# Optimization experiments

Measured on AMD Instinct MI355X. Metric: run time of the kernel, lower is better.

## Reference

```python
import jax, jax.numpy as jnp
import numpy as np

DIM = 128

def _layernorm(x, g, b, eps=1e-5):
    mu = jnp.mean(x, axis=-1, keepdims=True)
    var = jnp.var(x, axis=-1, keepdims=True)
    return (x - mu) * jax.lax.rsqrt(var + eps) * g + b

def setup_inputs() -> dict:
    key = jax.random.key(0)
    ks = jax.random.split(key, 12)
    B, T, O, d = 64, 1024, 128, DIM
    s = 1.0 / np.sqrt(d)
    s2 = 1.0 / np.sqrt(2 * d)
    return {
        "token_nodes": jax.random.normal(ks[0], (B, T, d), jnp.float32),
        "obj_nodes": jax.random.normal(ks[1], (B, O, d), jnp.float32),
        "attn_to_obj": jax.random.uniform(ks[2], (B, T, O), jnp.float32),
        "W_msg_o": jax.random.uniform(ks[3], (d, d), jnp.float32, -s, s),
        "b_msg_o": jnp.zeros((d,), jnp.float32),
        "W_msg_t": jax.random.uniform(ks[4], (d, d), jnp.float32, -s, s),
        "b_msg_t": jnp.zeros((d,), jnp.float32),
        "W_upd_t": jax.random.uniform(ks[5], (2 * d, d), jnp.float32, -s2, s2),
        "b_upd_t": jnp.zeros((d,), jnp.float32),
        "W_upd_o": jax.random.uniform(ks[6], (2 * d, d), jnp.float32, -s2, s2),
        "b_upd_o": jnp.zeros((d,), jnp.float32),
        "g_ln_t": jnp.ones((d,), jnp.float32),
        "beta_ln_t": jnp.zeros((d,), jnp.float32),
        "g_ln_o": jnp.ones((d,), jnp.float32),
        "beta_ln_o": jnp.zeros((d,), jnp.float32),
    }

def reference(token_nodes, obj_nodes, attn_to_obj,
              W_msg_o, b_msg_o, W_msg_t, b_msg_t,
              W_upd_t, b_upd_t, W_upd_o, b_upd_o,
              g_ln_t, beta_ln_t, g_ln_o, beta_ln_o):
    # messages from objects -> tokens
    msg_o = obj_nodes @ W_msg_o + b_msg_o                      # [B,O,d]
    agg_to_t = jnp.einsum('bto,bod->btd', attn_to_obj, msg_o)  # [B,T,d]
    # messages from tokens -> objects (transposed attention)
    msg_t = token_nodes @ W_msg_t + b_msg_t                    # [B,T,d]
    agg_to_o = jnp.einsum('bto,btd->bod', attn_to_obj, msg_t)  # [B,O,d]
    # fused update MLPs (dropout is identity in eval mode)
    new_t = jax.nn.relu(jnp.concatenate([token_nodes, agg_to_t], axis=-1) @ W_upd_t + b_upd_t)
    new_o = jax.nn.relu(jnp.concatenate([obj_nodes, agg_to_o], axis=-1) @ W_upd_o + b_upd_o)
    new_t = _layernorm(token_nodes + new_t, g_ln_t, beta_ln_t)
    new_o = _layernorm(obj_nodes + new_o, g_ln_o, beta_ln_o)
    return (new_t, new_o)
```

## Files before the change

### kernel.cpp

```cpp
#include <hip/hip_runtime.h>

typedef unsigned short u16;
typedef __attribute__((ext_vector_type(8))) short bf16x8;
typedef __attribute__((ext_vector_type(4))) float f32x4;

#define NB 64
#define NT 1024
#define NO 128
#define ND 128

__device__ __forceinline__ u16 f2bf(float f) {
    union { float f; unsigned u; } v; v.f = f;
    unsigned r = v.u + 0x7FFFu + ((v.u >> 16) & 1u);
    return (u16)(r >> 16);
}
__device__ __forceinline__ float bf2f(short s) {
    union { unsigned u; float f; } v; v.u = ((unsigned)(u16)s) << 16; return v.f;
}

__device__ __forceinline__ bf16x8 frag_from_f32(const float* p) {
    const float4 a = *reinterpret_cast<const float4*>(p);
    const float4 b = *reinterpret_cast<const float4*>(p + 4);
    bf16x8 r;
    r[0] = (short)f2bf(a.x); r[1] = (short)f2bf(a.y);
    r[2] = (short)f2bf(a.z); r[3] = (short)f2bf(a.w);
    r[4] = (short)f2bf(b.x); r[5] = (short)f2bf(b.y);
    r[6] = (short)f2bf(b.z); r[7] = (short)f2bf(b.w);
    return r;
}

__global__ void k_prep_weights(const float* __restrict__ Wmo, const float* __restrict__ Wmt,
                               const float* __restrict__ Wut, const float* __restrict__ Wuo,
                               u16* __restrict__ WmoT, u16* __restrict__ WmtT,
                               u16* __restrict__ WutT, u16* __restrict__ WuoT) {
    int idx = blockIdx.x * 256 + threadIdx.x;
    if (idx < 16384) {
        int k = idx >> 7, n = idx & 127;
        WmoT[n * 128 + k] = f2bf(Wmo[idx]);
    } else if (idx < 32768) {
        int i = idx - 16384; int k = i >> 7, n = i & 127;
        WmtT[n * 128 + k] = f2bf(Wmt[i]);
    } else if (idx < 65536) {
        int i = idx - 32768; int k = i >> 7, n = i & 127;
        WutT[n * 256 + (k ^ ((n & 7) << 3))] = f2bf(Wut[i]);
    } else if (idx < 98304) {
        int i = idx - 65536; int k = i >> 7, n = i & 127;
        WuoT[n * 256 + k] = f2bf(Wuo[i]);
    }
}

__global__ __launch_bounds__(256, 4)
void k_msg_o(const float* __restrict__ obj, const u16* __restrict__ WmoT,
             const float* __restrict__ bmo, u16* __restrict__ msg_oT) {
    __shared__ u16 lds_m[128][72];
    int bid = blockIdx.x;
    int rows_base = bid * 64;
    int l = threadIdx.x & 63, w = threadIdx.x >> 6;
    int l15 = l & 15, lk = (l >> 4) * 8, rsub = (l >> 4) * 4;
    int wrow = w * 16;
    int row0 = rows_base + wrow;

    f32x4 acc[8] = {};
    const float* xp = obj + (size_t)(row0 + l15) * 128;
#pragma unroll
    for (int kk = 0; kk < 4; kk++) {
        bf16x8 a = frag_from_f32(xp + kk * 32 + lk);
#pragma unroll
        for (int ct = 0; ct < 8; ct++) {
            bf16x8 bfr = *reinterpret_cast<const bf16x8*>(WmoT + (ct * 16 + l15) * 128 + kk * 32 + lk);
            acc[ct] = __builtin_amdgcn_mfma_f32_16x16x32_bf16(a, bfr, acc[ct], 0, 0, 0);
        }
    }
#pragma unroll
    for (int ct = 0; ct < 8; ct++) {
        int n = ct * 16 + l15;
        float bv = bmo[n];
        ushort4 pk;
        pk.x = f2bf(acc[ct][0] + bv);
        pk.y = f2bf(acc[ct][1] + bv);
        pk.z = f2bf(acc[ct][2] + bv);
        pk.w = f2bf(acc[ct][3] + bv);
        *reinterpret_cast<ushort4*>(&lds_m[n][wrow + rsub]) = pk;
    }
    __syncthreads();
    int n = threadIdx.x >> 1, h = threadIdx.x & 1;
    const u16* src = &lds_m[n][h * 32];
    int b = rows_base >> 7, o0 = rows_base & 127;
    u16* rowp = msg_oT + (size_t)(b * 128 + n) * 128;
#pragma unroll
    for (int i = 0; i < 4; i++) {
        int off = o0 + h * 32 + i * 8;
        *reinterpret_cast<bf16x8*>(rowp + (off ^ ((n & 7) << 3))) =
            *reinterpret_cast<const bf16x8*>(src + i * 8);
    }
}

__global__ __launch_bounds__(512, 2)
void k_P(const float* __restrict__ attn, const float* __restrict__ tok,
         u16* __restrict__ Psl, float* __restrict__ rs_part) {
    __shared__ u16 aT[128 * 256];
    __shared__ u16 dT[128 * 256];
    int b = blockIdx.x >> 2, ks = blockIdx.x & 3;
    int kb = ks * 256;
    int tid = threadIdx.x;

    int og = (tid & 31) * 4;
    int tg = tid >> 5;
    const float* asrc = attn + ((size_t)b * NT + kb) * 128;
    const float* tsrc = tok  + ((size_t)b * NT + kb) * 128;
#pragma unroll
    for (int half = 0; half < 2; half++) {
        const float* src = half ? tsrc : asrc;
        u16* buf = half ? dT : aT;
#pragma unroll
        for (int c = 0; c < 2; c++) {
            int t0 = tg * 16 + c * 8;
            f32x4 v[8];
#pragma unroll
            for (int i = 0; i < 8; i++)
                v[i] = *reinterpret_cast<const f32x4*>(src + (size_t)(t0 + i) * 128 + og);
            int gr = t0 >> 3;
#pragma unroll
            for (int j = 0; j < 4; j++) {
                int o = og + j;
                bf16x8 pk;
#pragma unroll
                for (int i = 0; i < 8; i++) pk[i] = (short)f2bf(v[i][j]);
                *reinterpret_cast<bf16x8*>(&buf[o * 256 + ((gr ^ (o & 31)) << 3)]) = pk;
            }
        }
    }
    __syncthreads();

    int l = tid & 63, w = tid >> 6;
    int l15 = l & 15, lk = (l >> 4) * 8, rsub = (l >> 4) * 4;
    int ro = w * 16 + l15;
    f32x4 acc[8] = {};
    float rsum = 0.f;
#pragma unroll
    for (int kk = 0; kk < 8; kk++) {
        int tt = kk * 32 + lk;
        bf16x8 a = *reinterpret_cast<const bf16x8*>(&aT[ro * 256 + (((tt >> 3) ^ (ro & 31)) << 3)]);
#pragma unroll
        for (int i = 0; i < 8; i++) rsum += bf2f(a[i]);
#pragma unroll
        for (int ct = 0; ct < 8; ct++) {
            int d = ct * 16 + l15;
            bf16x8 bf = *reinterpret_cast<const bf16x8*>(&dT[d * 256 + (((tt >> 3) ^ (d & 31)) << 3)]);
            acc[ct] = __builtin_amdgcn_mfma_f32_16x16x32_bf16(a, bf, acc[ct], 0, 0, 0);
        }
    }
    rsum += __shfl_xor(rsum, 16, 64);
    rsum += __shfl_xor(rsum, 32, 64);
    if (l < 16) rs_part[((size_t)ks * NB + b) * NO + w * 16 + l15] = rsum;
    u16* pout = Psl + (((size_t)(ks * NB + b)) * NO + w * 16) * ND;
#pragma unroll
    for (int ct = 0; ct < 8; ct++)
#pragma unroll
        for (int r = 0; r < 4; r++)
            pout[(size_t)(rsub + r) * ND + ct * 16 + l15] = f2bf(acc[ct][r]);
}

__global__ __launch_bounds__(256, 4)
void k_obj_final(const float* __restrict__ obj, const u16* __restrict__ Psl,
                 const float* __restrict__ rs_part, const u16* __restrict__ WmtT,
                 const float* __restrict__ bmt, const u16* __restrict__ WuoT,
                 const float* __restrict__ buo, const float* __restrict__ g,
                 const float* __restrict__ beta, float* __restrict__ out) {
    __shared__ u16 P_lds[32][136];
    __shared__ u16 agg_lds[32][136];
    __shared__ float rs_lds[32];
    __shared__ float part_s[32][2], part_sq[32][2];
    int bid = blockIdx.x;
    int b = bid >> 2, ot = bid & 3;
    int ob = ot * 32;
    int tid = threadIdx.x;
    {
        int row = tid >> 3, c0 = (tid & 7) * 16;
        float sm[16];
#pragma unroll
        for (int i = 0; i < 16; i++) sm[i] = 0.f;
#pragma unroll
        for (int ks = 0; ks < 4; ks++) {
            const u16* p = Psl + (((size_t)(ks * NB + b)) * NO + ob + row) * ND + c0;
            bf16x8 v0 = *reinterpret_cast<const bf16x8*>(p);
            bf16x8 v1 = *reinterpret_cast<const bf16x8*>(p + 8);
#pragma unroll
            for (int i = 0; i < 8; i++) { sm[i] += bf2f(v0[i]); sm[8 + i] += bf2f(v1[i]); }
        }
#pragma unroll
        for (int j = 0; j < 4; j++) {
            ushort4 pk;
            pk.x = f2bf(sm[j * 4 + 0]); pk.y = f2bf(sm[j * 4 + 1]);
            pk.z = f2bf(sm[j * 4 + 2]); pk.w = f2bf(sm[j * 4 + 3]);
            *reinterpret_cast<ushort4*>(&P_lds[row][c0 + j * 4]) = pk;
        }
        if (tid < 32) {
            float r = 0.f;
#pragma unroll
            for (int ks = 0; ks < 4; ks++) r += rs_part[((size_t)ks * NB + b) * NO + ob + tid];
            rs_lds[tid] = r;
        }
    }
    __syncthreads();
    int l = tid & 63, w = tid >> 6;
    int l15 = l & 15, lk = (l >> 4) * 8, rsub = (l >> 4) * 4;
    int wr = (w & 1) * 16, wc = (w >> 1) * 64;
    f32x4 agg[4] = {};
#pragma unroll
    for (int kk = 0; kk < 4; kk++) {
        bf16x8 a = *reinterpret_cast<const bf16x8*>(&P_lds[wr + l15][kk * 32 + lk]);
#pragma unroll
        for (int ct = 0; ct < 4; ct++) {
            bf16x8 bf = *reinterpret_cast<const bf16x8*>(WmtT + (wc + ct * 16 + l15) * 128 + kk * 32 + lk);
            agg[ct] = __builtin_amdgcn_mfma_f32_16x16x32_bf16(a, bf, agg[ct], 0, 0, 0);
        }
    }
#pragma unroll
    for (int ct = 0; ct < 4; ct++) {
        int n = wc + ct * 16 + l15;
        float bb = bmt[n];
#pragma unroll
        for (int r = 0; r < 4; r++) {
            float v = agg[ct][r] + rs_lds[wr + rsub + r] * bb;
            agg_lds[wr + rsub + r][n] = f2bf(v);
        }
    }
    __syncthreads();
    f32x4 accm[4] = {};
    const float* objp = obj + ((size_t)(b * NO) + ob + wr + l15) * ND;
#pragma unroll
    for (int kk = 0; kk < 8; kk++) {
        int k0 = kk * 32;
        bf16x8 a = (k0 < 128) ? frag_from_f32(objp + k0 + lk)
                              : *reinterpret_cast<const bf16x8*>(&agg_lds[wr + l15][k0 - 128 + lk]);
#pragma unroll
        for (int ct = 0; ct < 4; ct++) {
            bf16x8 bf = *reinterpret_cast<const bf16x8*>(WuoT + (wc + ct * 16 + l15) * 256 + k0 + lk);
            accm[ct] = __builtin_amdgcn_mfma_f32_16x16x32_bf16(a, bf, accm[ct], 0, 0, 0);
        }
    }
    const float* objr = obj + ((size_t)(b * NO) + ob) * ND;
    float s[4] = {0.f, 0.f, 0.f, 0.f}, sq[4] = {0.f, 0.f, 0.f, 0.f};
#pragma unroll
    for (int ct = 0; ct < 4; ct++) {
        int n = wc + ct * 16 + l15;
        float bv = buo[n];
#pragma unroll
        for (int r = 0; r < 4; r++) {
            int lr = wr + rsub + r;
            float v = objr[(size_t)lr * ND + n] + fmaxf(accm[ct][r] + bv, 0.f);
            accm[ct][r] = v;
            s[r] += v;
            sq[r] += v * v;
        }
    }
#pragma unroll
    for (int ofs = 1; ofs < 16; ofs <<= 1) {
#pragma unroll
        for (int r = 0; r < 4; r++) {
            s[r]  += __shfl_xor(s[r], ofs, 64);
            sq[r] += __shfl_xor(sq[r], ofs, 64);
        }
    }
    if (l15 < 4) {
        float sv = (l15 == 0) ? s[0] : (l15 == 1) ? s[1] : (l15 == 2) ? s[2] : s[3];
        float qv = (l15 == 0) ? sq[0] : (l15 == 1) ? sq[1] : (l15 == 2) ? sq[2] : sq[3];
        part_s[wr + rsub + l15][w >> 1] = sv;
        part_sq[wr + rsub + l15][w >> 1] = qv;
    }
    __syncthreads();
    float mu[4], rstd[4];
#pragma unroll
    for (int r = 0; r < 4; r++) {
        int lr = wr + rsub + r;
        float st = part_s[lr][0] + part_s[lr][1];
        float qt = part_sq[lr][0] + part_sq[lr][1];
        mu[r] = st * (1.f / 128.f);
        rstd[r] = rsqrtf(qt * (1.f / 128.f) - mu[r] * mu[r] + 1e-5f);
    }
#pragma unroll
    for (int ct = 0; ct < 4; ct++) {
        int n = wc + ct * 16 + l15;
        float gn = g[n], bn = beta[n];
#pragma unroll
        for (int r = 0; r < 4; r++) {
            int lr = wr + rsub + r;
            out[((size_t)(b * NO) + ob + lr) * ND + n] = (accm[ct][r] - mu[r]) * rstd[r] * gn + bn;
        }
    }
}

__global__ __launch_bounds__(512, 2)
void k_token_update(const float* __restrict__ tok, const float* __restrict__ attn,
                    const u16* __restrict__ msg_oT, const u16* __restrict__ WutT,
                    const float* __restrict__ bupd, const float* __restrict__ g,
                    const float* __restrict__ beta, float* __restrict__ out) {
    __shared__ u16 msg_lds[16384];
    __shared__ u16 wut_lds[32768];
    __shared__ u16 agg_b[8][16][136];
    int b = blockIdx.x >> 2, bq = blockIdx.x & 3;
    int tid = threadIdx.x;
    {
        const u16* msrc = msg_oT + (size_t)b * 16384;
#pragma unroll
        for (int i = 0; i < 4; i++) {
            int idx = (i * 512 + tid) * 8;
            *reinterpret_cast<bf16x8*>(&msg_lds[idx]) = *reinterpret_cast<const bf16x8*>(msrc + idx);
        }
#pragma unroll
        for (int i = 0; i < 8; i++) {
            int idx = (i * 512 + tid) * 8;
            *reinterpret_cast<bf16x8*>(&wut_lds[idx]) = *reinterpret_cast<const bf16x8*>(WutT + idx);
        }
    }
    __syncthreads();
    int l = tid & 63, w = tid >> 6;
    int l15 = l & 15, lk = (l >> 4) * 8, rsub = (l >> 4) * 4;

#pragma unroll
    for (int pass = 0; pass < 2; pass++) {
        int trow = bq * 256 + pass * 128 + w * 16;
        size_t rbase = (size_t)b * NT + trow;

        const float* aF = attn + (rbase + l15) * NO;
        bf16x8 af[4];
#pragma unroll
        for (int kk = 0; kk < 4; kk++)
            af[kk] = frag_from_f32(aF + kk * 32 + lk);
        f32x4 acc[8] = {};
#pragma unroll
        for (int kk = 0; kk < 4; kk++) {
#pragma unroll
            for (int ct = 0; ct < 8; ct++) {
                int n = ct * 16 + l15;
                bf16x8 bf = *reinterpret_cast<const bf16x8*>(
                    &msg_lds[n * 128 + ((kk * 32 + lk) ^ ((n & 7) << 3))]);
                acc[ct] = __builtin_amdgcn_mfma_f32_16x16x32_bf16(af[kk], bf, acc[ct], 0, 0, 0);
            }
        }
#pragma unroll
        for (int ct = 0; ct < 8; ct++) {
            int n = ct * 16 + l15;
#pragma unroll
            for (int r = 0; r < 4; r++)
                agg_b[w][rsub + r][n] = f2bf(acc[ct][r]);
        }
        asm volatile("s_waitcnt lgkmcnt(0)" ::: "memory");
        __builtin_amdgcn_sched_barrier(0);
        const float* tokp = tok + (rbase + l15) * ND;
        bf16x8 am[8];
#pragma unroll
        for (int kk = 0; kk < 4; kk++)
            am[kk] = frag_from_f32(tokp + kk * 32 + lk);
#pragma unroll
        for (int kk = 0; kk < 4; kk++)
            am[4 + kk] = *reinterpret_cast<const bf16x8*>(&agg_b[w][l15][kk * 32 + lk]);
        f32x4 accm[8] = {};
#pragma unroll
        for (int kk = 0; kk < 8; kk++) {
#pragma unroll
            for (int ct = 0; ct < 8; ct++) {
                int n = ct * 16 + l15;
                bf16x8 bf = *reinterpret_cast<const bf16x8*>(
                    &wut_lds[n * 256 + ((kk * 32 + lk) ^ ((n & 7) << 3))]);
                accm[ct] = __builtin_amdgcn_mfma_f32_16x16x32_bf16(am[kk], bf, accm[ct], 0, 0, 0);
            }
        }
        const float* tokr = tok + rbase * ND;
        float s[4] = {0.f, 0.f, 0.f, 0.f}, sq[4] = {0.f, 0.f, 0.f, 0.f};
#pragma unroll
        for (int ct = 0; ct < 8; ct++) {
            int n = ct * 16 + l15;
            float bv = bupd[n];
#pragma unroll
            for (int r = 0; r < 4; r++) {
                float v = tokr[(size_t)(rsub + r) * ND + n] + fmaxf(accm[ct][r] + bv, 0.f);
                accm[ct][r] = v;
                s[r] += v;
                sq[r] += v * v;
            }
        }
#pragma unroll
        for (int ofs = 1; ofs < 16; ofs <<= 1) {
#pragma unroll
            for (int r = 0; r < 4; r++) {
                s[r]  += __shfl_xor(s[r], ofs, 64);
                sq[r] += __shfl_xor(sq[r], ofs, 64);
            }
        }
        float mu[4], rstd[4];
#pragma unroll
        for (int r = 0; r < 4; r++) {
            mu[r] = s[r] * (1.f / 128.f);
            rstd[r] = rsqrtf(sq[r] * (1.f / 128.f) - mu[r] * mu[r] + 1e-5f);
        }
#pragma unroll
        for (int ct = 0; ct < 8; ct++) {
            int n = ct * 16 + l15;
            float gn = g[n], bn = beta[n];
#pragma unroll
            for (int r = 0; r < 4; r++)
                out[(rbase + rsub + r) * ND + n] = (accm[ct][r] - mu[r]) * rstd[r] * gn + bn;
        }
    }
}

extern "C" void kernel_launch(void* const* d_in, const int* in_sizes, int n_in,
                              void* d_out, int out_size, void* d_ws, size_t ws_size,
                              hipStream_t stream) {
    const float* tok  = (const float*)d_in[0];
    const float* obj  = (const float*)d_in[1];
    const float* attn = (const float*)d_in[2];
    const float* Wmo  = (const float*)d_in[3];
    const float* bmo  = (const float*)d_in[4];
    const float* Wmt  = (const float*)d_in[5];
    const float* bmt  = (const float*)d_in[6];
    const float* Wut  = (const float*)d_in[7];
    const float* but  = (const float*)d_in[8];
    const float* Wuo  = (const float*)d_in[9];
    const float* buo  = (const float*)d_in[10];
    const float* gt   = (const float*)d_in[11];
    const float* bt   = (const float*)d_in[12];
    const float* go   = (const float*)d_in[13];
    const float* bo   = (const float*)d_in[14];
    float* out = (float*)d_out;

    u16* ws = (u16*)d_ws;
    u16* msg_oT = ws;
    u16* WmoT   = msg_oT + 1048576;
    u16* WmtT   = WmoT + 16384;
    u16* WutT   = WmtT + 16384;
    u16* WuoT   = WutT + 32768;
    u16* Psl    = WuoT + 32768;
    float* rs_part = (float*)(Psl + 4194304);

    k_prep_weights<<<dim3(384), dim3(256), 0, stream>>>(Wmo, Wmt, Wut, Wuo, WmoT, WmtT, WutT, WuoT);
    k_msg_o<<<dim3(128), dim3(256), 0, stream>>>(obj, WmoT, bmo, msg_oT);
    k_P<<<dim3(256), dim3(512), 0, stream>>>(attn, tok, Psl, rs_part);
    k_token_update<<<dim3(256), dim3(512), 0, stream>>>(tok, attn, msg_oT, WutT, but, gt, bt, out);
    k_obj_final<<<dim3(256), dim3(256), 0, stream>>>(obj, Psl, rs_part, WmtT, bmt, WuoT, buo, go, bo,
                                                     out + (size_t)NB * NT * ND);
}
```

Baseline: 65.40 us.

## Fuse weight prep into msg_o kernel and chunk k_P LDS staging

Removes the separate weight-conversion kernel. Each k_msg_o block now converts Wmo into a shared-memory transposed tile, and the blocks together convert the other three weights, saving one launch. k_P now stages its 256-token slice in two 128-token chunks with half the LDS, so launch bounds can request 4 blocks per SM for more occupancy. The cost is an extra barrier per chunk and redundant per-block Wmo conversion work.

```diff
diff --git a/kernel.cpp b/kernel.cpp
--- a/kernel.cpp
+++ b/kernel.cpp
@@ -29,33 +29,40 @@
     return r;
 }
 
-__global__ void k_prep_weights(const float* __restrict__ Wmo, const float* __restrict__ Wmt,
-                               const float* __restrict__ Wut, const float* __restrict__ Wuo,
-                               u16* __restrict__ WmoT, u16* __restrict__ WmtT,
-                               u16* __restrict__ WutT, u16* __restrict__ WuoT) {
-    int idx = blockIdx.x * 256 + threadIdx.x;
-    if (idx < 16384) {
-        int k = idx >> 7, n = idx & 127;
-        WmoT[n * 128 + k] = f2bf(Wmo[idx]);
-    } else if (idx < 32768) {
-        int i = idx - 16384; int k = i >> 7, n = i & 127;
-        WmtT[n * 128 + k] = f2bf(Wmt[i]);
-    } else if (idx < 65536) {
-        int i = idx - 32768; int k = i >> 7, n = i & 127;
-        WutT[n * 256 + (k ^ ((n & 7) << 3))] = f2bf(Wut[i]);
-    } else if (idx < 98304) {
-        int i = idx - 65536; int k = i >> 7, n = i & 127;
-        WuoT[n * 256 + k] = f2bf(Wuo[i]);
-    }
-}
-
 __global__ __launch_bounds__(256, 4)
-void k_msg_o(const float* __restrict__ obj, const u16* __restrict__ WmoT,
-             const float* __restrict__ bmo, u16* __restrict__ msg_oT) {
+void k_msg_o(const float* __restrict__ obj, const float* __restrict__ Wmo,
+             const float* __restrict__ bmo,
+             const float* __restrict__ Wmt, const float* __restrict__ Wut,
+             const float* __restrict__ Wuo,
+             u16* __restrict__ msg_oT, u16* __restrict__ WmtT,
+             u16* __restrict__ WutT, u16* __restrict__ WuoT) {
+    __shared__ u16 wT[128][136];
     __shared__ u16 lds_m[128][72];
     int bid = blockIdx.x;
+    int tid = threadIdx.x;
+
+    for (int idx = bid * 256 + tid; idx < 81920; idx += 32768) {
+        if (idx < 16384) {
+            int k = idx >> 7, n = idx & 127;
+            WmtT[n * 128 + k] = f2bf(Wmt[idx]);
+        } else if (idx < 49152) {
+            int i2 = idx - 16384; int k = i2 >> 7, n = i2 & 127;
+            WutT[n * 256 + (k ^ ((n & 7) << 3))] = f2bf(Wut[i2]);
+        } else {
+            int i2 = idx - 49152; int k = i2 >> 7, n = i2 & 127;
+            WuoT[n * 256 + k] = f2bf(Wuo[i2]);
+        }
+    }
+#pragma unroll
+    for (int i = 0; i < 64; i++) {
+        int idx = i * 256 + tid;
+        int k = idx >> 7, n = idx & 127;
+        wT[n][k] = f2bf(Wmo[idx]);
+    }
+    __syncthreads();
+
     int rows_base = bid * 64;
-    int l = threadIdx.x & 63, w = threadIdx.x >> 6;
+    int l = tid & 63, w = tid >> 6;
     int l15 = l & 15, lk = (l >> 4) * 8, rsub = (l >> 4) * 4;
     int wrow = w * 16;
     int row0 = rows_base + wrow;
@@ -67,7 +74,7 @@
         bf16x8 a = frag_from_f32(xp + kk * 32 + lk);
 #pragma unroll
         for (int ct = 0; ct < 8; ct++) {
-            bf16x8 bfr = *reinterpret_cast<const bf16x8*>(WmoT + (ct * 16 + l15) * 128 + kk * 32 + lk);
+            bf16x8 bfr = *reinterpret_cast<const bf16x8*>(&wT[ct * 16 + l15][kk * 32 + lk]);
             acc[ct] = __builtin_amdgcn_mfma_f32_16x16x32_bf16(a, bfr, acc[ct], 0, 0, 0);
         }
     }
@@ -83,7 +90,7 @@
         *reinterpret_cast<ushort4*>(&lds_m[n][wrow + rsub]) = pk;
     }
     __syncthreads();
-    int n = threadIdx.x >> 1, h = threadIdx.x & 1;
+    int n = tid >> 1, h = tid & 1;
     const u16* src = &lds_m[n][h * 32];
     int b = rows_base >> 7, o0 = rows_base & 127;
     u16* rowp = msg_oT + (size_t)(b * 128 + n) * 128;
@@ -95,26 +102,32 @@
     }
 }
 
-__global__ __launch_bounds__(512, 2)
+__global__ __launch_bounds__(512, 4)
 void k_P(const float* __restrict__ attn, const float* __restrict__ tok,
          u16* __restrict__ Psl, float* __restrict__ rs_part) {
-    __shared__ u16 aT[128 * 256];
-    __shared__ u16 dT[128 * 256];
+    __shared__ u16 aT[128 * 128];
+    __shared__ u16 dT[128 * 128];
     int b = blockIdx.x >> 2, ks = blockIdx.x & 3;
-    int kb = ks * 256;
     int tid = threadIdx.x;
-
+    int l = tid & 63, w = tid >> 6;
+    int l15 = l & 15, lk = (l >> 4) * 8, rsub = (l >> 4) * 4;
+    int ro = w * 16 + l15;
     int og = (tid & 31) * 4;
     int tg = tid >> 5;
-    const float* asrc = attn + ((size_t)b * NT + kb) * 128;
-    const float* tsrc = tok  + ((size_t)b * NT + kb) * 128;
-#pragma unroll
-    for (int half = 0; half < 2; half++) {
-        const float* src = half ? tsrc : asrc;
-        u16* buf = half ? dT : aT;
-#pragma unroll
-        for (int c = 0; c < 2; c++) {
-            int t0 = tg * 16 + c * 8;
+
+    f32x4 acc[8] = {};
+    float rsum = 0.f;
+#pragma unroll
+    for (int c = 0; c < 2; c++) {
+        int kb = ks * 256 + c * 128;
+        const float* asrc = attn + ((size_t)b * NT + kb) * 128;
+        const float* tsrc = tok  + ((size_t)b * NT + kb) * 128;
+        if (c) __syncthreads();
+#pragma unroll
+        for (int half = 0; half < 2; half++) {
+            const float* src = half ? tsrc : asrc;
+            u16* buf = half ? dT : aT;
+            int t0 = tg * 8;
             f32x4 v[8];
 #pragma unroll
             for (int i = 0; i < 8; i++)
@@ -126,28 +139,24 @@
                 bf16x8 pk;
 #pragma unroll
                 for (int i = 0; i < 8; i++) pk[i] = (short)f2bf(v[i][j]);
-                *reinterpret_cast<bf16x8*>(&buf[o * 256 + ((gr ^ (o & 31)) << 3)]) = pk;
-            }
-        }
-    }
-    __syncthreads();
-
-    int l = tid & 63, w = tid >> 6;
-    int l15 = l & 15, lk = (l >> 4) * 8, rsub = (l >> 4) * 4;
-    int ro = w * 16 + l15;
-    f32x4 acc[8] = {};
-    float rsum = 0.f;
-#pragma unroll
-    for (int kk = 0; kk < 8; kk++) {
-        int tt = kk * 32 + lk;
-        bf16x8 a = *reinterpret_cast<const bf16x8*>(&aT[ro * 256 + (((tt >> 3) ^ (ro & 31)) << 3)]);
-#pragma unroll
-        for (int i = 0; i < 8; i++) rsum += bf2f(a[i]);
-#pragma unroll
-        for (int ct = 0; ct < 8; ct++) {
-            int d = ct * 16 + l15;
-            bf16x8 bf = *reinterpret_cast<const bf16x8*>(&dT[d * 256 + (((tt >> 3) ^ (d & 31)) << 3)]);
-            acc[ct] = __builtin_amdgcn_mfma_f32_16x16x32_bf16(a, bf, acc[ct], 0, 0, 0);
+                *reinterpret_cast<bf16x8*>(&buf[o * 128 + ((gr ^ (o & 15)) << 3)]) = pk;
+            }
+        }
+        __syncthreads();
+#pragma unroll
+        for (int kk = 0; kk < 4; kk++) {
+            int tt = kk * 32 + lk;
+            bf16x8 a = *reinterpret_cast<const bf16x8*>(
+                &aT[ro * 128 + (((tt >> 3) ^ (ro & 15)) << 3)]);
+#pragma unroll
+            for (int i = 0; i < 8; i++) rsum += bf2f(a[i]);
+#pragma unroll
+            for (int ct = 0; ct < 8; ct++) {
+                int d = ct * 16 + l15;
+                bf16x8 bf = *reinterpret_cast<const bf16x8*>(
+                    &dT[d * 128 + (((tt >> 3) ^ (d & 15)) << 3)]);
+                acc[ct] = __builtin_amdgcn_mfma_f32_16x16x32_bf16(a, bf, acc[ct], 0, 0, 0);
+            }
         }
     }
     rsum += __shfl_xor(rsum, 16, 64);
@@ -428,15 +437,14 @@
 
     u16* ws = (u16*)d_ws;
     u16* msg_oT = ws;
-    u16* WmoT   = msg_oT + 1048576;
-    u16* WmtT   = WmoT + 16384;
+    u16* WmtT   = msg_oT + 1048576;
     u16* WutT   = WmtT + 16384;
     u16* WuoT   = WutT + 32768;
     u16* Psl    = WuoT + 32768;
     float* rs_part = (float*)(Psl + 4194304);
 
-    k_prep_weights<<<dim3(384), dim3(256), 0, stream>>>(Wmo, Wmt, Wut, Wuo, WmoT, WmtT, WutT, WuoT);
-    k_msg_o<<<dim3(128), dim3(256), 0, stream>>>(obj, WmoT, bmo, msg_oT);
+    k_msg_o<<<dim3(128), dim3(256), 0, stream>>>(obj, Wmo, bmo, Wmt, Wut, Wuo,
+                                                 msg_oT, WmtT, WutT, WuoT);
     k_P<<<dim3(256), dim3(512), 0, stream>>>(attn, tok, Psl, rs_part);
     k_token_update<<<dim3(256), dim3(512), 0, stream>>>(tok, attn, msg_oT, WutT, but, gt, bt, out);
     k_obj_final<<<dim3(256), dim3(256), 0, stream>>>(obj, Psl, rs_part, WmtT, bmt, WuoT, buo, go, bo,
```

Result: faster. 61.44 us (-6.1%).
